# Performance work log

Hardware: AMD Instinct MI355X
Metric: run time of the kernel (lower is better)

Reference implementation:

```python
import jax, jax.numpy as jnp
import numpy as np

NUM_NEURONS = 65536
T_STEPS = 1024
V_TH = 1.0
V_RESET = 0.0
TAU = 20.0
DT = 1.0


def setup_inputs() -> dict:
    key = jax.random.key(0)
    input_current = jax.random.normal(key, (T_STEPS, NUM_NEURONS), dtype=jnp.float32)
    return {"input_current": input_current}


def reference(input_current) -> jnp.ndarray:
    """LIF recurrence. The original loops over the batch axis while each
    neuron object carries membrane potential V across rows, so the batch
    axis is sequential (time). Vectorized over neurons, lax.scan over time.

    V <- V + dt/tau * (-(V - V_reset) + I)
    spike = V >= V_th ; V <- V_reset where spiked
    """
    alpha = jnp.float32(DT / TAU)

    def step(V, I):
        V = V + alpha * (V_RESET - V + I)
        spike = V >= V_TH
        V = jnp.where(spike, jnp.float32(V_RESET), V)
        return V, spike.astype(jnp.float32)

    V0 = jnp.full((input_current.shape[1],), V_RESET, dtype=jnp.float32)
    _, spikes = jax.lax.scan(step, V0, input_current)
    return spikes  # (T, N) binary float32
```

## Files before the change

### kernel.cpp

```cpp
#include <hip/hip_runtime.h>


#define T_STEPS 1024
#define N NUM_NEURONS
#define NUM_NEURONS 65536
#define BLOCK 256
#define U 16

__global__ __launch_bounds__(BLOCK) void lif_kernel(const float* __restrict__ in,
                                                    float* __restrict__ out) {
    const int gid = blockIdx.x * BLOCK + threadIdx.x;
    constexpr float alpha = 0.05f;
    constexpr float vth = 1.0f;

    float V = 0.0f;
    const float* __restrict__ p = in + gid;
    float* __restrict__ q = out + gid;

    float I[U], J[U];

#pragma unroll
    for (int u = 0; u < U; ++u) I[u] = p[(size_t)u * N];

    for (int t = 0; t < T_STEPS - U; t += U) {
#pragma unroll
        for (int u = 0; u < U; ++u) J[u] = p[(size_t)(t + U + u) * N];
#pragma unroll
        for (int u = 0; u < U; ++u) {
            V = V + alpha * (I[u] - V);
            float s = (V >= vth) ? 1.0f : 0.0f;
            V = (V >= vth) ? 0.0f : V;
            __builtin_nontemporal_store(s, q + (size_t)(t + u) * N);
        }
#pragma unroll
        for (int u = 0; u < U; ++u) I[u] = J[u];
    }

#pragma unroll
    for (int u = 0; u < U; ++u) {
        V = V + alpha * (I[u] - V);
        float s = (V >= vth) ? 1.0f : 0.0f;
        V = (V >= vth) ? 0.0f : V;
        __builtin_nontemporal_store(s, q + (size_t)(T_STEPS - U + u) * N);
    }
}

extern "C" void kernel_launch(void* const* d_in, const int* in_sizes, int n_in,
                              void* d_out, int out_size, void* d_ws, size_t ws_size,
                              hipStream_t stream) {
    const float* in = (const float*)d_in[0];
    float* out = (float*)d_out;
    lif_kernel<<<NUM_NEURONS / BLOCK, BLOCK, 0, stream>>>(in, out);
}
```

Measured before the change: 425.7 us.

## Buffer spike bits in shared memory and write outputs after recurrence

Packs each chunk of 32 spike flags into a bitmask held in LDS during the time recurrence, then emits all float spike outputs in a separate store phase. This separates the input-read stream from the output-write stream and doubles the prefetch unroll. It costs 32 KB of LDS per block, which may reduce occupancy, and removes the per-thread overlap of loads and stores.

```diff
diff --git a/kernel.cpp b/kernel.cpp
--- a/kernel.cpp
+++ b/kernel.cpp
@@ -2,46 +2,67 @@
 
 
 #define T_STEPS 1024
+#define NUM_NEURONS 65536
 #define N NUM_NEURONS
-#define NUM_NEURONS 65536
 #define BLOCK 256
-#define U 16
+#define U 32
+#define NCHUNK (T_STEPS / U)
 
 __global__ __launch_bounds__(BLOCK) void lif_kernel(const float* __restrict__ in,
                                                     float* __restrict__ out) {
-    const int gid = blockIdx.x * BLOCK + threadIdx.x;
+    __shared__ unsigned int words[NCHUNK][BLOCK];
+
+    const int tid = threadIdx.x;
+    const int gid = blockIdx.x * BLOCK + tid;
     constexpr float alpha = 0.05f;
     constexpr float vth = 1.0f;
 
+    const float* __restrict__ p = in + gid;
+
     float V = 0.0f;
-    const float* __restrict__ p = in + gid;
-    float* __restrict__ q = out + gid;
-
     float I[U], J[U];
 
 #pragma unroll
     for (int u = 0; u < U; ++u) I[u] = p[(size_t)u * N];
 
-    for (int t = 0; t < T_STEPS - U; t += U) {
+    for (int k = 0; k < NCHUNK - 1; ++k) {
 #pragma unroll
-        for (int u = 0; u < U; ++u) J[u] = p[(size_t)(t + U + u) * N];
+        for (int u = 0; u < U; ++u) J[u] = p[(size_t)((k + 1) * U + u) * N];
+
+        unsigned int w = 0u;
 #pragma unroll
         for (int u = 0; u < U; ++u) {
             V = V + alpha * (I[u] - V);
-            float s = (V >= vth) ? 1.0f : 0.0f;
-            V = (V >= vth) ? 0.0f : V;
-            __builtin_nontemporal_store(s, q + (size_t)(t + u) * N);
+            const bool s = (V >= vth);
+            w |= s ? (1u << u) : 0u;
+            V = s ? 0.0f : V;
         }
+        words[k][tid] = w;
+
 #pragma unroll
         for (int u = 0; u < U; ++u) I[u] = J[u];
     }
 
+    {
+        unsigned int w = 0u;
 #pragma unroll
-    for (int u = 0; u < U; ++u) {
-        V = V + alpha * (I[u] - V);
-        float s = (V >= vth) ? 1.0f : 0.0f;
-        V = (V >= vth) ? 0.0f : V;
-        __builtin_nontemporal_store(s, q + (size_t)(T_STEPS - U + u) * N);
+        for (int u = 0; u < U; ++u) {
+            V = V + alpha * (I[u] - V);
+            const bool s = (V >= vth);
+            w |= s ? (1u << u) : 0u;
+            V = s ? 0.0f : V;
+        }
+        words[NCHUNK - 1][tid] = w;
+    }
+
+    float* __restrict__ q = out + gid;
+    for (int k = 0; k < NCHUNK; ++k) {
+        const unsigned int w = words[k][tid];
+#pragma unroll
+        for (int u = 0; u < U; ++u) {
+            const float s = (w & (1u << u)) ? 1.0f : 0.0f;
+            __builtin_nontemporal_store(s, q + (size_t)(k * U + u) * N);
+        }
     }
 }
 
```

After: 435.9 us. +2.4%, slower.
